# Kernel optimization log

Hardware: AMD Instinct MI355X
Metric: run time of the kernel (lower is better)

## Reference

```python
import jax, jax.numpy as jnp
import numpy as np

N, T, H, KQ, V = 8, 256, 8, 128, 32  # batch, seq (Tq=Tk=T), heads, kq_dim, value_dim(=latent_dim)
SCALE = 1.0 / np.sqrt(KQ)


def setup_inputs() -> dict:
    k = jax.random.split(jax.random.key(0), 10)
    w = 0.05
    return {
        "value": jax.random.normal(k[0], (N, T, V), dtype=jnp.float32),
        "key": jax.random.normal(k[1], (N, T, KQ), dtype=jnp.float32),
        "query": jax.random.normal(k[2], (N, T, KQ), dtype=jnp.float32),
        "mask": jax.random.randint(k[3], (N, T, V), 0, 2, dtype=jnp.int32),
        # attn_linear[0]: query proj, attn_linear[1]: key proj (torch Linear: y = x @ W.T + b)
        "Wq": jax.random.normal(k[4], (H * KQ, KQ), dtype=jnp.float32) * w,
        "bq": jax.random.normal(k[5], (H * KQ,), dtype=jnp.float32) * w,
        "Wk": jax.random.normal(k[6], (H * KQ, KQ), dtype=jnp.float32) * w,
        "bk": jax.random.normal(k[7], (H * KQ,), dtype=jnp.float32) * w,
        "Wo": jax.random.normal(k[8], (V, H * V), dtype=jnp.float32) * w,  # attn_out: Linear(ld*H, ld), ld == V
        "bo": jax.random.normal(k[9], (V,), dtype=jnp.float32) * w,
    }


def reference(value, key, query, mask, Wq, bq, Wk, bk, Wo, bo):
    n, t, vdim = value.shape
    nq, tq, _ = query.shape
    nk, tk, _ = key.shape
    h = Wq.shape[0] // query.shape[-1]
    kq = query.shape[-1]

    # per-head projections: (N, H, T, KQ)
    hq = (query @ Wq.T + bq).reshape(nq, tq, h, kq).transpose(0, 2, 1, 3)
    hk = (key @ Wk.T + bk).reshape(nk, tk, h, kq).transpose(0, 2, 1, 3)

    # scores: (N, H, Tq, Tk), then broadcast per value-dim -> (N, H, Tq, Tk, V)
    scores = jnp.einsum("nhqd,nhkd->nhqk", hq, hk) * jnp.asarray(SCALE, value.dtype)
    scores = jnp.broadcast_to(scores[..., None], (n, h, tq, tk, vdim))

    # mask (N, Tk, V): mask[i,t,d]==0 means value[i,t,d] unobserved
    m = mask[:, None, None, :, :]  # (N,1,1,Tk,V)
    scores = jnp.where(m == 0, jnp.asarray(-1e9, scores.dtype), scores)

    p_attn = jax.nn.softmax(scores, axis=-2)  # softmax over Tk, per value-dim

    # weighted sum over keys: (N, H, Tq, V) -> (N, Tq, H*V)
    out = jnp.einsum("nhqkv,nkv->nqhv", p_attn, value).reshape(n, tq, h * vdim)
    out_rep = out @ Wo.T + bo  # (N, Tq, ld)
    return out_rep, p_attn
```

## Files before the change

kernel.cpp:

```cpp
#include <hip/hip_runtime.h>

#define N_ 8
#define T_ 256
#define H_ 8
#define KQ_ 128
#define V_ 32

typedef float f32x4 __attribute__((ext_vector_type(4)));

__global__ __launch_bounds__(256) void proj_kernel(
    const float* __restrict__ query, const float* __restrict__ key,
    const float* __restrict__ Wq, const float* __restrict__ bq,
    const float* __restrict__ Wk, const float* __restrict__ bk,
    float* __restrict__ hqT, float* __restrict__ hkT)
{
  int b = blockIdx.x;
  int dh = b & 1;
  int h  = (b >> 1) & 7;
  int n  = (b >> 4) & 7;
  int proj = (b >> 7) & 1;
  const float* src  = proj ? key : query;
  const float* W    = proj ? Wk  : Wq;
  const float* bias = proj ? bk  : bq;
  float* dst        = proj ? hkT : hqT;
  int d0 = dh * 64;

  __shared__ float qs[256 * 36];
  __shared__ float ws[64 * 36];

  int tl   = threadIdx.x & 31;
  int dsub = threadIdx.x >> 5;
  const float* qsrc = src + (size_t)n * T_ * KQ_;
  const float* wsrc = W + (size_t)(h * KQ_ + d0) * KQ_;

  float acc[8][8];
#pragma unroll
  for (int it = 0; it < 8; ++it)
#pragma unroll
    for (int dd = 0; dd < 8; ++dd) acc[it][dd] = 0.f;

  for (int kc = 0; kc < 4; ++kc) {
    if (kc) __syncthreads();
    {
      int r = threadIdx.x >> 3, c4 = (threadIdx.x & 7) * 4;
#pragma unroll
      for (int rep = 0; rep < 8; ++rep) {
        int row = r + rep * 32;
        *(float4*)&qs[row * 36 + c4] =
            *(const float4*)&qsrc[(size_t)row * KQ_ + kc * 32 + c4];
      }
#pragma unroll
      for (int rep = 0; rep < 2; ++rep) {
        int row = r + rep * 32;
        *(float4*)&ws[row * 36 + c4] =
            *(const float4*)&wsrc[(size_t)row * KQ_ + kc * 32 + c4];
      }
    }
    __syncthreads();

#pragma unroll 2
    for (int j0 = 0; j0 < 32; j0 += 4) {
      float4 qv[8];
#pragma unroll
      for (int it = 0; it < 8; ++it)
        qv[it] = *(const float4*)&qs[(tl + 32 * it) * 36 + j0];
#pragma unroll
      for (int dd = 0; dd < 8; ++dd) {
        float4 w4 = *(const float4*)&ws[(dsub * 8 + dd) * 36 + j0];
#pragma unroll
        for (int it = 0; it < 8; ++it) {
          acc[it][dd] = fmaf(qv[it].x, w4.x, acc[it][dd]);
          acc[it][dd] = fmaf(qv[it].y, w4.y, acc[it][dd]);
          acc[it][dd] = fmaf(qv[it].z, w4.z, acc[it][dd]);
          acc[it][dd] = fmaf(qv[it].w, w4.w, acc[it][dd]);
        }
      }
    }
  }

#pragma unroll
  for (int dd = 0; dd < 8; ++dd) {
    int d = d0 + dsub * 8 + dd;
    float bb = bias[h * KQ_ + d];
    size_t base = (((size_t)n * H_ + h) * KQ_ + d) * T_;
#pragma unroll
    for (int it = 0; it < 8; ++it)
      dst[base + it * 32 + tl] = acc[it][dd] + bb;
  }
}

__global__ __launch_bounds__(64) void attn_kernel(
    const float* __restrict__ hqT, const float* __restrict__ hkT,
    const int* __restrict__ mask, const float* __restrict__ value,
    float* __restrict__ e_ws, float* __restrict__ inv_ws,
    float* __restrict__ out_ws)
{
  const float SCALE = 0.08838834764831845f;
  int b = blockIdx.x;
  int q0 = (b & 31) * 8;
  int h  = (b >> 5) & 7;
  int n  = b >> 8;
  int l  = threadIdx.x;
  int row0 = (n * H_ + h) * T_ + q0;

  __shared__ float hq_s[KQ_ * 12];
  __shared__ float e_s[T_ * 8];

  const float* hqbase = hqT + ((size_t)n * H_ + h) * KQ_ * T_;
  const float* hkbase = hkT + ((size_t)n * H_ + h) * KQ_ * T_;

#pragma unroll
  for (int rep = 0; rep < 16; ++rep) {
    int i = l + 64 * rep;
    int j = i >> 3, qq = i & 7;
    hq_s[j * 12 + qq] = hqbase[(size_t)j * T_ + q0 + qq];
  }
  __syncthreads();

  float acc[4][8];
#pragma unroll
  for (int i = 0; i < 4; ++i)
#pragma unroll
    for (int qq = 0; qq < 8; ++qq) acc[i][qq] = 0.f;

#pragma unroll 4
  for (int j = 0; j < KQ_; ++j) {
    float hk0 = hkbase[(size_t)j * T_ + l];
    float hk1 = hkbase[(size_t)j * T_ + l + 64];
    float hk2 = hkbase[(size_t)j * T_ + l + 128];
    float hk3 = hkbase[(size_t)j * T_ + l + 192];
    float4 a0 = *(const float4*)&hq_s[j * 12];
    float4 a1 = *(const float4*)&hq_s[j * 12 + 4];
    acc[0][0] = fmaf(a0.x, hk0, acc[0][0]); acc[0][1] = fmaf(a0.y, hk0, acc[0][1]);
    acc[0][2] = fmaf(a0.z, hk0, acc[0][2]); acc[0][3] = fmaf(a0.w, hk0, acc[0][3]);
    acc[0][4] = fmaf(a1.x, hk0, acc[0][4]); acc[0][5] = fmaf(a1.y, hk0, acc[0][5]);
    acc[0][6] = fmaf(a1.z, hk0, acc[0][6]); acc[0][7] = fmaf(a1.w, hk0, acc[0][7]);
    acc[1][0] = fmaf(a0.x, hk1, acc[1][0]); acc[1][1] = fmaf(a0.y, hk1, acc[1][1]);
    acc[1][2] = fmaf(a0.z, hk1, acc[1][2]); acc[1][3] = fmaf(a0.w, hk1, acc[1][3]);
    acc[1][4] = fmaf(a1.x, hk1, acc[1][4]); acc[1][5] = fmaf(a1.y, hk1, acc[1][5]);
    acc[1][6] = fmaf(a1.z, hk1, acc[1][6]); acc[1][7] = fmaf(a1.w, hk1, acc[1][7]);
    acc[2][0] = fmaf(a0.x, hk2, acc[2][0]); acc[2][1] = fmaf(a0.y, hk2, acc[2][1]);
    acc[2][2] = fmaf(a0.z, hk2, acc[2][2]); acc[2][3] = fmaf(a0.w, hk2, acc[2][3]);
    acc[2][4] = fmaf(a1.x, hk2, acc[2][4]); acc[2][5] = fmaf(a1.y, hk2, acc[2][5]);
    acc[2][6] = fmaf(a1.z, hk2, acc[2][6]); acc[2][7] = fmaf(a1.w, hk2, acc[2][7]);
    acc[3][0] = fmaf(a0.x, hk3, acc[3][0]); acc[3][1] = fmaf(a0.y, hk3, acc[3][1]);
    acc[3][2] = fmaf(a0.z, hk3, acc[3][2]); acc[3][3] = fmaf(a0.w, hk3, acc[3][3]);
    acc[3][4] = fmaf(a1.x, hk3, acc[3][4]); acc[3][5] = fmaf(a1.y, hk3, acc[3][5]);
    acc[3][6] = fmaf(a1.z, hk3, acc[3][6]); acc[3][7] = fmaf(a1.w, hk3, acc[3][7]);
  }

  float ev[4][8];
  {
#pragma unroll
    for (int qq = 0; qq < 8; ++qq) {
      float m = fmaxf(fmaxf(acc[0][qq] * SCALE, acc[1][qq] * SCALE),
                      fmaxf(acc[2][qq] * SCALE, acc[3][qq] * SCALE));
      for (int off = 32; off >= 1; off >>= 1)
        m = fmaxf(m, __shfl_xor(m, off, 64));
#pragma unroll
      for (int i = 0; i < 4; ++i)
        ev[i][qq] = __expf(acc[i][qq] * SCALE - m);
    }
  }
#pragma unroll
  for (int i = 0; i < 4; ++i) {
#pragma unroll
    for (int qq = 0; qq < 8; ++qq)
      e_ws[(size_t)(row0 + qq) * T_ + l + 64 * i] = ev[i][qq];
    int k = l + 64 * i;
    *(f32x4*)&e_s[k * 8]     = f32x4{ev[i][0], ev[i][1], ev[i][2], ev[i][3]};
    *(f32x4*)&e_s[k * 8 + 4] = f32x4{ev[i][4], ev[i][5], ev[i][6], ev[i][7]};
  }
  __syncthreads();

  const int*   mrow = mask  + (size_t)n * T_ * V_;
  const float* vrow = value + (size_t)n * T_ * V_;
  int v = l & 31, kh = l >> 5;
  float s8[8], o8[8];
#pragma unroll
  for (int qq = 0; qq < 8; ++qq) { s8[qq] = 0.f; o8[qq] = 0.f; }
#pragma unroll 4
  for (int i = 0; i < 128; ++i) {
    int k = kh * 128 + i;
    float mf = (float)mrow[k * V_ + v];
    float vv = vrow[k * V_ + v];
    float4 e0 = *(const float4*)&e_s[k * 8];
    float4 e1 = *(const float4*)&e_s[k * 8 + 4];
    float p;
    p = e0.x * mf; s8[0] += p; o8[0] = fmaf(p, vv, o8[0]);
    p = e0.y * mf; s8[1] += p; o8[1] = fmaf(p, vv, o8[1]);
    p = e0.z * mf; s8[2] += p; o8[2] = fmaf(p, vv, o8[2]);
    p = e0.w * mf; s8[3] += p; o8[3] = fmaf(p, vv, o8[3]);
    p = e1.x * mf; s8[4] += p; o8[4] = fmaf(p, vv, o8[4]);
    p = e1.y * mf; s8[5] += p; o8[5] = fmaf(p, vv, o8[5]);
    p = e1.z * mf; s8[6] += p; o8[6] = fmaf(p, vv, o8[6]);
    p = e1.w * mf; s8[7] += p; o8[7] = fmaf(p, vv, o8[7]);
  }
#pragma unroll
  for (int qq = 0; qq < 8; ++qq) {
    s8[qq] += __shfl_xor(s8[qq], 32, 64);
    o8[qq] += __shfl_xor(o8[qq], 32, 64);
  }
  if (kh == 0) {
#pragma unroll
    for (int qq = 0; qq < 8; ++qq) {
      float inv = 1.0f / s8[qq];
      inv_ws[(size_t)(row0 + qq) * V_ + v] = inv;
      out_ws[(((size_t)n * T_ + q0 + qq) * H_ + h) * V_ + v] = o8[qq] * inv;
    }
  }
}

__global__ __launch_bounds__(256) void pwrite_kernel(
    const float* __restrict__ e_ws, const float* __restrict__ inv_ws,
    const int* __restrict__ mask, float* __restrict__ p_out)
{
  int b = blockIdx.x;
  int row0 = b * 4;
  int n = row0 >> 11;
  const int* mrow = mask + (size_t)n * T_ * V_;
  int t = threadIdx.x;
  int v0 = (t & 7) * 4;
  int kbase = t >> 3;

  float4 iv[4];
  const float* erow[4];
  f32x4* dst4[4];
#pragma unroll
  for (int qq = 0; qq < 4; ++qq) {
    int row = row0 + qq;
    iv[qq]   = *(const float4*)&inv_ws[(size_t)row * V_ + v0];
    erow[qq] = e_ws + (size_t)row * T_;
    dst4[qq] = (f32x4*)p_out + (size_t)row * 2048;
  }

#pragma unroll
  for (int rep = 0; rep < 8; ++rep) {
    int k = rep * 32 + kbase;
    const int4 m4 = *(const int4*)&mrow[k * V_ + v0];
    float fx = (float)m4.x, fy = (float)m4.y, fz = (float)m4.z, fw = (float)m4.w;
#pragma unroll
    for (int qq = 0; qq < 4; ++qq) {
      float e = erow[qq][k];
      f32x4 pv;
      pv.x = e * fx * iv[qq].x;
      pv.y = e * fy * iv[qq].y;
      pv.z = e * fz * iv[qq].z;
      pv.w = e * fw * iv[qq].w;
      __builtin_nontemporal_store(pv, &dst4[qq][rep * 256 + t]);
    }
  }
}

__global__ __launch_bounds__(256) void outproj_kernel(
    const float* __restrict__ out_ws, const float* __restrict__ Wo,
    const float* __restrict__ bo, float* __restrict__ out_rep)
{
  __shared__ float wot[256 * 33];
  __shared__ float rows_s[4 * 256];
  __shared__ float red[4 * 32];
  int r0 = blockIdx.x * 4;
  for (int i = threadIdx.x; i < 32 * 256; i += 256) {
    int o = i >> 8, c = i & 255;
    wot[c * 33 + o] = Wo[i];
  }
  for (int i = threadIdx.x; i < 4 * 256; i += 256)
    rows_s[i] = out_ws[(size_t)r0 * 256 + i];
  __syncthreads();
  int o  = threadIdx.x & 31;
  int rr = (threadIdx.x >> 5) & 3;
  int kh = threadIdx.x >> 7;
  int cb = kh * 128;
  float acc = 0.f;
#pragma unroll 4
  for (int c = 0; c < 128; ++c)
    acc = fmaf(rows_s[rr * 256 + cb + c], wot[(cb + c) * 33 + o], acc);
  if (kh == 1) red[rr * 32 + o] = acc;
  __syncthreads();
  if (kh == 0)
    out_rep[(size_t)(r0 + rr) * 32 + o] = acc + red[rr * 32 + o] + bo[o];
}

extern "C" void kernel_launch(void* const* d_in, const int* in_sizes, int n_in,
                              void* d_out, int out_size, void* d_ws, size_t ws_size,
                              hipStream_t stream) {
  const float* value = (const float*)d_in[0];
  const float* key   = (const float*)d_in[1];
  const float* query = (const float*)d_in[2];
  const int*   mask  = (const int*)d_in[3];
  const float* Wq = (const float*)d_in[4];
  const float* bq = (const float*)d_in[5];
  const float* Wk = (const float*)d_in[6];
  const float* bk = (const float*)d_in[7];
  const float* Wo = (const float*)d_in[8];
  const float* bo = (const float*)d_in[9];

  float* out_rep = (float*)d_out;
  float* p_out   = (float*)d_out + (size_t)N_ * T_ * V_;

  float* hqT    = (float*)d_ws;
  float* hkT    = hqT    + (size_t)N_ * H_ * KQ_ * T_;
  float* out_ws = hkT    + (size_t)N_ * H_ * KQ_ * T_;
  float* e_ws   = out_ws + (size_t)N_ * T_ * H_ * V_;
  float* inv_ws = e_ws   + (size_t)N_ * H_ * T_ * T_;

  hipLaunchKernelGGL(proj_kernel, dim3(256), dim3(256), 0, stream,
                     query, key, Wq, bq, Wk, bk, hqT, hkT);
  hipLaunchKernelGGL(attn_kernel, dim3(2048), dim3(64), 0, stream,
                     hqT, hkT, mask, value, e_ws, inv_ws, out_ws);
  hipLaunchKernelGGL(pwrite_kernel, dim3(4096), dim3(256), 0, stream,
                     e_ws, inv_ws, mask, p_out);
  hipLaunchKernelGGL(outproj_kernel, dim3(512), dim3(256), 0, stream,
                     out_ws, Wo, bo, out_rep);
}
```

Measured before the change: 170.4 us.

## Fuse probability write into attention kernel, drop e/inv workspace round trip

The separate pwrite kernel is removed and the attention kernel now writes the normalized probability tensor directly, using the exp values already held in shared memory and the inverse sums kept in a new shared array. This avoids writing and re-reading the N*H*T*T exp workspace and the inverse-sum workspace through global memory, and saves one kernel launch. In exchange, each 64-thread attention block now issues the large 64 MB p_attn store itself (8 rows x 256 keys x 32 values), so there are fewer threads in flight to saturate write bandwidth than the old 256-thread pwrite grid had.

```diff
diff --git a/kernel.cpp b/kernel.cpp
--- a/kernel.cpp
+++ b/kernel.cpp
@@ -92,8 +92,7 @@
 __global__ __launch_bounds__(64) void attn_kernel(
     const float* __restrict__ hqT, const float* __restrict__ hkT,
     const int* __restrict__ mask, const float* __restrict__ value,
-    float* __restrict__ e_ws, float* __restrict__ inv_ws,
-    float* __restrict__ out_ws)
+    float* __restrict__ p_out, float* __restrict__ out_ws)
 {
   const float SCALE = 0.08838834764831845f;
   int b = blockIdx.x;
@@ -105,6 +104,7 @@
 
   __shared__ float hq_s[KQ_ * 12];
   __shared__ float e_s[T_ * 8];
+  __shared__ float inv_s[8 * 32];
 
   const float* hqbase = hqT + ((size_t)n * H_ + h) * KQ_ * T_;
   const float* hkbase = hkT + ((size_t)n * H_ + h) * KQ_ * T_;
@@ -149,7 +149,6 @@
     acc[3][6] = fmaf(a1.z, hk3, acc[3][6]); acc[3][7] = fmaf(a1.w, hk3, acc[3][7]);
   }
 
-  float ev[4][8];
   {
 #pragma unroll
     for (int qq = 0; qq < 8; ++qq) {
@@ -159,17 +158,14 @@
         m = fmaxf(m, __shfl_xor(m, off, 64));
 #pragma unroll
       for (int i = 0; i < 4; ++i)
-        ev[i][qq] = __expf(acc[i][qq] * SCALE - m);
+        acc[i][qq] = __expf(acc[i][qq] * SCALE - m);
     }
   }
 #pragma unroll
   for (int i = 0; i < 4; ++i) {
-#pragma unroll
-    for (int qq = 0; qq < 8; ++qq)
-      e_ws[(size_t)(row0 + qq) * T_ + l + 64 * i] = ev[i][qq];
     int k = l + 64 * i;
-    *(f32x4*)&e_s[k * 8]     = f32x4{ev[i][0], ev[i][1], ev[i][2], ev[i][3]};
-    *(f32x4*)&e_s[k * 8 + 4] = f32x4{ev[i][4], ev[i][5], ev[i][6], ev[i][7]};
+    *(f32x4*)&e_s[k * 8]     = f32x4{acc[i][0], acc[i][1], acc[i][2], acc[i][3]};
+    *(f32x4*)&e_s[k * 8 + 4] = f32x4{acc[i][4], acc[i][5], acc[i][6], acc[i][7]};
   }
   __syncthreads();
 
@@ -205,49 +201,38 @@
 #pragma unroll
     for (int qq = 0; qq < 8; ++qq) {
       float inv = 1.0f / s8[qq];
-      inv_ws[(size_t)(row0 + qq) * V_ + v] = inv;
+      inv_s[qq * 32 + v] = inv;
       out_ws[(((size_t)n * T_ + q0 + qq) * H_ + h) * V_ + v] = o8[qq] * inv;
     }
   }
-}
-
-__global__ __launch_bounds__(256) void pwrite_kernel(
-    const float* __restrict__ e_ws, const float* __restrict__ inv_ws,
-    const int* __restrict__ mask, float* __restrict__ p_out)
-{
-  int b = blockIdx.x;
-  int row0 = b * 4;
-  int n = row0 >> 11;
-  const int* mrow = mask + (size_t)n * T_ * V_;
-  int t = threadIdx.x;
-  int v0 = (t & 7) * 4;
-  int kbase = t >> 3;
-
-  float4 iv[4];
-  const float* erow[4];
-  f32x4* dst4[4];
-#pragma unroll
-  for (int qq = 0; qq < 4; ++qq) {
-    int row = row0 + qq;
-    iv[qq]   = *(const float4*)&inv_ws[(size_t)row * V_ + v0];
-    erow[qq] = e_ws + (size_t)row * T_;
-    dst4[qq] = (f32x4*)p_out + (size_t)row * 2048;
-  }
-
-#pragma unroll
-  for (int rep = 0; rep < 8; ++rep) {
-    int k = rep * 32 + kbase;
-    const int4 m4 = *(const int4*)&mrow[k * V_ + v0];
-    float fx = (float)m4.x, fy = (float)m4.y, fz = (float)m4.z, fw = (float)m4.w;
-#pragma unroll
-    for (int qq = 0; qq < 4; ++qq) {
-      float e = erow[qq][k];
-      f32x4 pv;
-      pv.x = e * fx * iv[qq].x;
-      pv.y = e * fy * iv[qq].y;
-      pv.z = e * fz * iv[qq].z;
-      pv.w = e * fw * iv[qq].w;
-      __builtin_nontemporal_store(pv, &dst4[qq][rep * 256 + t]);
+  __syncthreads();
+
+  {
+    int v0 = (l & 7) * 4;
+    f32x4 iv[8];
+#pragma unroll
+    for (int qq = 0; qq < 8; ++qq)
+      iv[qq] = *(const f32x4*)&inv_s[qq * 32 + v0];
+    f32x4* pbase = (f32x4*)p_out + (size_t)row0 * 2048;
+
+#pragma unroll 4
+    for (int rep = 0; rep < 32; ++rep) {
+      int e4 = rep * 64 + l;
+      int k  = rep * 8 + (l >> 3);
+      const int4 m4 = *(const int4*)&mrow[k * V_ + v0];
+      float fx = (float)m4.x, fy = (float)m4.y, fz = (float)m4.z, fw = (float)m4.w;
+      f32x4 e0 = *(const f32x4*)&e_s[k * 8];
+      f32x4 e1 = *(const f32x4*)&e_s[k * 8 + 4];
+      float e[8] = {e0.x, e0.y, e0.z, e0.w, e1.x, e1.y, e1.z, e1.w};
+#pragma unroll
+      for (int qq = 0; qq < 8; ++qq) {
+        f32x4 pv;
+        pv.x = e[qq] * fx * iv[qq].x;
+        pv.y = e[qq] * fy * iv[qq].y;
+        pv.z = e[qq] * fz * iv[qq].z;
+        pv.w = e[qq] * fw * iv[qq].w;
+        __builtin_nontemporal_store(pv, &pbase[(size_t)qq * 2048 + e4]);
+      }
     }
   }
 }
@@ -299,17 +284,13 @@
   float* p_out   = (float*)d_out + (size_t)N_ * T_ * V_;
 
   float* hqT    = (float*)d_ws;
-  float* hkT    = hqT    + (size_t)N_ * H_ * KQ_ * T_;
-  float* out_ws = hkT    + (size_t)N_ * H_ * KQ_ * T_;
-  float* e_ws   = out_ws + (size_t)N_ * T_ * H_ * V_;
-  float* inv_ws = e_ws   + (size_t)N_ * H_ * T_ * T_;
+  float* hkT    = hqT + (size_t)N_ * H_ * KQ_ * T_;
+  float* out_ws = hkT + (size_t)N_ * H_ * KQ_ * T_;
 
   hipLaunchKernelGGL(proj_kernel, dim3(256), dim3(256), 0, stream,
                      query, key, Wq, bq, Wk, bk, hqT, hkT);
   hipLaunchKernelGGL(attn_kernel, dim3(2048), dim3(64), 0, stream,
-                     hqT, hkT, mask, value, e_ws, inv_ws, out_ws);
-  hipLaunchKernelGGL(pwrite_kernel, dim3(4096), dim3(256), 0, stream,
-                     e_ws, inv_ws, mask, p_out);
+                     hqT, hkT, mask, value, p_out, out_ws);
   hipLaunchKernelGGL(outproj_kernel, dim3(512), dim3(256), 0, stream,
                      out_ws, Wo, bo, out_rep);
 }
```

New measurement: 157.9 us. 7.3% less time.
